# Optimization experiments

Measured on AMD Instinct MI355X. Metric: run time of the kernel, lower is better.

Reference implementation:

```python
import jax, jax.numpy as jnp
import numpy as np

B, H, W, C = 8, 64, 64, 512
DQK = C // 8  # query/key channel dim from Conv2D(filters//8, 1)


def setup_inputs() -> dict:
    key = jax.random.key(0)
    ks = jax.random.split(key, 8)
    s_in = 1.0 / np.sqrt(C)
    x = jax.random.normal(ks[0], (B, H, W, C), dtype=jnp.float32)
    Wq = jax.random.normal(ks[1], (C, DQK), dtype=jnp.float32) * s_in
    bq = jnp.zeros((DQK,), dtype=jnp.float32)
    Wk = jax.random.normal(ks[2], (C, DQK), dtype=jnp.float32) * s_in
    bk = jnp.zeros((DQK,), dtype=jnp.float32)
    Wv = jax.random.normal(ks[3], (C, C), dtype=jnp.float32) * s_in
    bv = jnp.zeros((C,), dtype=jnp.float32)
    # gamma initialized to zeros in the original, but use a nonzero value so
    # the attention branch actually contributes to the output/gradients.
    gamma = jnp.ones((1,), dtype=jnp.float32) * 0.5
    return {"x": x, "Wq": Wq, "bq": bq, "Wk": Wk, "bk": bk,
            "Wv": Wv, "bv": bv, "gamma": gamma}


def reference(x, Wq, bq, Wk, bk, Wv, bv, gamma):
    b, h, w, c = x.shape
    n = h * w  # spatial_size
    xf = x.reshape(b, n, c)
    # 1x1 convs == per-pixel channel matmuls
    q = xf @ Wq + bq            # [B, N, C//8]
    k = xf @ Wk + bk            # [B, N, C//8]
    v = xf @ Wv + bv            # [B, N, C]
    # Dot(axes=-1): attn[b,i,j] = sum_d q[b,i,d] * k[b,j,d]
    attn = jnp.einsum('bid,bjd->bij', q, k)
    attn = jax.nn.softmax(attn, axis=-1)
    # Dot(axes=-2): out[b,j,c] = sum_i attn[b,i,j] * v[b,i,c]  (note transpose)
    out = jnp.einsum('bij,bic->bjc', attn, v)
    out = out.reshape(b, h, w, c)
    return gamma * out + x
```

## Files before the change

### kernel.cpp

```cpp
#include <hip/hip_runtime.h>
#include <hip/hip_bf16.h>
#include <cstdio>

typedef unsigned short u16;
typedef __attribute__((ext_vector_type(4))) float f32x4;
typedef __attribute__((ext_vector_type(8))) short s16x8;

__device__ __forceinline__ u16 bf16b(float f) {
  union { float f; unsigned u; } c; c.f = f;
  unsigned u = c.u;
  return (u16)((u + 0x7FFFu + ((u >> 16) & 1u)) >> 16);
}

__device__ __forceinline__ void load16(const void* g, void* l) {
  __builtin_amdgcn_global_load_lds(
      (const __attribute__((address_space(1))) void*)g,
      (__attribute__((address_space(3))) void*)l, 16, 0, 0);
}

#define BARV() asm volatile("s_waitcnt vmcnt(0) lgkmcnt(0)\n\ts_barrier" ::: "memory")
#define BAR() asm volatile("s_waitcnt lgkmcnt(0)\n\ts_barrier" ::: "memory")


__global__ __launch_bounds__(256) void cvt_all_k(const float* __restrict__ x,
                                                 const float* __restrict__ Wq,
                                                 const float* __restrict__ Wk,
                                                 const float* __restrict__ Wv,
                                                 u16* __restrict__ xb,
                                                 u16* __restrict__ Wcat) {
  int bid = blockIdx.x;
  if (bid < 16384) {
    long i = ((long)bid * 256 + threadIdx.x) * 4;
    float4 f = *(const float4*)&x[i];
    unsigned lo = (unsigned)bf16b(f.x) | ((unsigned)bf16b(f.y) << 16);
    unsigned hi = (unsigned)bf16b(f.z) | ((unsigned)bf16b(f.w) << 16);
    uint2 v; v.x = lo; v.y = hi;
    *(uint2*)&xb[i] = v;
  } else {
    int idx = (bid - 16384) * 256 + threadIdx.x;
    int nn = idx >> 9, k = idx & 511;
    float v;
    if (nn < 64)       v = Wq[k * 64 + nn];
    else if (nn < 128) v = Wk[k * 64 + (nn - 64)];
    else               v = Wv[k * 512 + (nn - 128)];
    Wcat[idx] = bf16b(v);
  }
}

__global__ __launch_bounds__(256, 2) void projGemm(
    const u16* __restrict__ A, const u16* __restrict__ B,
    u16* __restrict__ Qb, u16* __restrict__ Kb, u16* __restrict__ Vt,
    const float* __restrict__ bq, const float* __restrict__ bk,
    const float* __restrict__ bv) {
  constexpr int BM = 128, BN = 128, FM = 4, FN = 4;
  __shared__ __align__(16) u16 At[BM * 64];
  __shared__ __align__(16) u16 Bt[BN * 64];
  const int tid = threadIdx.x;
  const int lane = tid & 63, w = tid >> 6;
  const int wr = w >> 1, wc = w & 1;
  const int l15 = lane & 15, lhi = lane >> 4;
  const long m0 = (long)blockIdx.x * BM;
  const long n0 = (long)blockIdx.y * BN;

  f32x4 acc[FM][FN] = {};

  for (int k0 = 0; k0 < 512; k0 += 64) {
#pragma unroll
    for (int it = 0; it < 8; ++it) {
      int q = it * 256 + tid;
      if (q < BM * 8) {
        int row = q >> 3, c8 = q & 7;
        load16(A + (m0 + row) * 512 + k0 + c8 * 8, &At[q * 8]);
      } else {
        int q2 = q - BM * 8;
        int row = q2 >> 3, c8 = q2 & 7;
        load16(B + (n0 + row) * 512 + k0 + c8 * 8, &Bt[q2 * 8]);
      }
    }
    __syncthreads();
#pragma unroll
    for (int kk = 0; kk < 64; kk += 32) {
      s16x8 af[FM], bf[FN];
#pragma unroll
      for (int i = 0; i < FM; ++i)
        af[i] = *(const s16x8*)&At[(wr * 64 + i * 16 + l15) * 64 + kk + lhi * 8];
#pragma unroll
      for (int j = 0; j < FN; ++j)
        bf[j] = *(const s16x8*)&Bt[(wc * 64 + j * 16 + l15) * 64 + kk + lhi * 8];
#pragma unroll
      for (int i = 0; i < FM; ++i)
#pragma unroll
        for (int j = 0; j < FN; ++j)
          acc[i][j] = __builtin_amdgcn_mfma_f32_16x16x32_bf16(af[i], bf[j],
                                                              acc[i][j], 0, 0, 0);
    }
    __syncthreads();
  }

#pragma unroll
  for (int i = 0; i < FM; ++i) {
#pragma unroll
    for (int j = 0; j < FN; ++j) {
      long mm = m0 + wr * 64 + i * 16 + lhi * 4;
      long nn = n0 + wc * 64 + j * 16 + l15;
      if (nn < 64) {
        float bb = bq[nn];
#pragma unroll
        for (int r = 0; r < 4; ++r)
          Qb[(mm + r) * 64 + nn] = bf16b(acc[i][j][r] + bb);
      } else if (nn < 128) {
        float bb = bk[nn - 64];
#pragma unroll
        for (int r = 0; r < 4; ++r)
          Kb[(mm + r) * 64 + nn - 64] = bf16b(acc[i][j][r] + bb);
      } else {
        long c = nn - 128;
        float bb = bv[c];
        unsigned u01 = (unsigned)bf16b(acc[i][j][0] + bb) |
                       ((unsigned)bf16b(acc[i][j][1] + bb) << 16);
        unsigned u23 = (unsigned)bf16b(acc[i][j][2] + bb) |
                       ((unsigned)bf16b(acc[i][j][3] + bb) << 16);
        uint2 u; u.x = u01; u.y = u23;
        *(uint2*)&Vt[(mm >> 12) * 512 * 4096 + c * 4096 + (mm & 4095)] = u;
      }
    }
  }
}

__global__ __launch_bounds__(256, 2) void stats_k(const u16* __restrict__ Qb,
                                                  const u16* __restrict__ Kb,
                                                  float* __restrict__ m_part,
                                                  float* __restrict__ l_part) {
  const int b = blockIdx.z, jc = blockIdx.y;
  const long i0 = (long)blockIdx.x * 128;
  const u16* Q = Qb + (long)b * 4096 * 64;
  const u16* Kp = Kb + (long)b * 4096 * 64;
  __shared__ __align__(16) u16 Qt[128 * 64];
  __shared__ __align__(16) u16 Kt[128 * 64];
  const int tid = threadIdx.x, lane = tid & 63, w = tid >> 6;
  const int l15 = lane & 15, lhi = lane >> 4;

#pragma unroll
  for (int it = 0; it < 4; ++it) {
    int q = it * 256 + tid;
    int row = q >> 3, c8 = q & 7;
    load16(Q + (i0 + row) * 64 + c8 * 8, &Qt[q * 8]);
  }

  float mrun[2][4], lrun[2][4];
#pragma unroll
  for (int i = 0; i < 2; ++i)
#pragma unroll
    for (int r = 0; r < 4; ++r) { mrun[i][r] = -1e30f; lrun[i][r] = 0.f; }

  for (int jt = 0; jt < 8; ++jt) {
    long j0 = (long)jc * 1024 + jt * 128;
#pragma unroll
    for (int it = 0; it < 4; ++it) {
      int q = it * 256 + tid;
      int row = q >> 3, c8 = q & 7;
      load16(Kp + (j0 + row) * 64 + c8 * 8, &Kt[q * 8]);
    }
    __syncthreads();
    f32x4 acc[2][8] = {};
#pragma unroll
    for (int kk = 0; kk < 64; kk += 32) {
      s16x8 af[2], bf[8];
#pragma unroll
      for (int i = 0; i < 2; ++i)
        af[i] = *(const s16x8*)&Qt[(w * 32 + i * 16 + l15) * 64 + kk + lhi * 8];
#pragma unroll
      for (int j = 0; j < 8; ++j)
        bf[j] = *(const s16x8*)&Kt[(j * 16 + l15) * 64 + kk + lhi * 8];
#pragma unroll
      for (int i = 0; i < 2; ++i)
#pragma unroll
        for (int j = 0; j < 8; ++j)
          acc[i][j] = __builtin_amdgcn_mfma_f32_16x16x32_bf16(af[i], bf[j],
                                                              acc[i][j], 0, 0, 0);
    }
#pragma unroll
    for (int i = 0; i < 2; ++i)
#pragma unroll
      for (int r = 0; r < 4; ++r) {
        float tm = acc[i][0][r];
#pragma unroll
        for (int j = 1; j < 8; ++j) tm = fmaxf(tm, acc[i][j][r]);
        float mo = mrun[i][r];
        float mn = fmaxf(mo, tm);
        float s = 0.f;
#pragma unroll
        for (int j = 0; j < 8; ++j) s += __expf(acc[i][j][r] - mn);
        lrun[i][r] = lrun[i][r] * __expf(mo - mn) + s;
        mrun[i][r] = mn;
      }
    __syncthreads();
  }

#pragma unroll
  for (int i = 0; i < 2; ++i)
#pragma unroll
    for (int r = 0; r < 4; ++r) {
      float m = mrun[i][r], l = lrun[i][r];
#pragma unroll
      for (int d = 1; d < 16; d <<= 1) {
        float mo = __shfl_xor(m, d);
        float lo = __shfl_xor(l, d);
        float mn = fmaxf(m, mo);
        l = l * __expf(m - mn) + lo * __expf(mo - mn);
        m = mn;
      }
      if (l15 == 0) {
        long ig = i0 + w * 32 + i * 16 + lhi * 4 + r;
        long idx = ((long)(b * 4 + jc)) * 4096 + ig;
        m_part[idx] = m;
        l_part[idx] = l;
      }
    }
}

__global__ __launch_bounds__(256) void merge_k(const float* __restrict__ m_part,
                                               const float* __restrict__ l_part,
                                               float* __restrict__ mfin,
                                               float* __restrict__ linv) {
  int idx = blockIdx.x * 256 + threadIdx.x;
  int b = idx >> 12, i = idx & 4095;
  float m = -1e30f, l = 0.f;
#pragma unroll
  for (int jc = 0; jc < 4; ++jc) {
    long o = ((long)(b * 4 + jc)) * 4096 + i;
    float mp = m_part[o], lp = l_part[o];
    float mn = fmaxf(m, mp);
    l = l * __expf(m - mn) + lp * __expf(mp - mn);
    m = mn;
  }
  mfin[idx] = m;
  linv[idx] = 1.0f / l;
}

__global__ __launch_bounds__(512, 2) void fusedPV(
    const u16* __restrict__ Qb, const u16* __restrict__ Kb,
    const u16* __restrict__ Vt, const float* __restrict__ mfin,
    const float* __restrict__ lnv, const float* __restrict__ x,
    const float* __restrict__ gamma, float* __restrict__ out) {
  __shared__ __align__(16) u16 Qc[2][64 * 64];
  __shared__ __align__(16) u16 Vc[2][256 * 64];
  __shared__ __align__(16) u16 Pl[256 * 64];
  const int tid = threadIdx.x, lane = tid & 63, w = tid >> 6;
  const int l15 = lane & 15, lhi = lane >> 4;
  const int wi = w & 1, wj = w >> 1, wc = w & 1;
  const int s = blockIdx.x + 16 * (blockIdx.y + 2 * blockIdx.z);
  const int pi = (s & 7) * 32 + (s >> 3);
  const int b = pi >> 5;
  const long j0 = (long)(pi & 15) * 256;
  const long c0 = (long)((pi >> 4) & 1) * 256;
  const u16* Qg = Qb + (long)b * 4096 * 64;
  const u16* Kg = Kb + (long)b * 4096 * 64;
  const u16* Vg = Vt + (long)b * 512 * 4096;
  const float* mg = mfin + (long)b * 4096;
  const float* lg = lnv + (long)b * 4096;

#pragma unroll
  for (int p = 0; p < 4; ++p) {
    int q = p * 512 + tid;
    int r = q >> 3, col = q & 7, cg = col ^ (r & 7);
    load16(Kg + (j0 + r) * 64 + cg * 8, (char*)Pl + r * 128 + col * 16);
  }
  BARV();
  s16x8 kf[4][2];
#pragma unroll
  for (int fj = 0; fj < 4; ++fj)
#pragma unroll
    for (int kx = 0; kx < 2; ++kx) {
      int r = wj * 64 + fj * 16 + l15;
      kf[fj][kx] = *(const s16x8*)((const char*)Pl + r * 128 +
                                   (((kx * 32 + lhi * 8) * 2) ^ ((r & 7) << 4)));
    }
  __syncthreads();

  {
    int r = tid >> 3, col = tid & 7, cg = col ^ (r & 7);
    load16(Qg + (long)r * 64 + cg * 8, (char*)&Qc[0][0] + r * 128 + col * 16);
#pragma unroll
    for (int p = 0; p < 4; ++p) {
      int q = p * 512 + tid;
      int r2 = q >> 3, c2 = q & 7, cg2 = c2 ^ (r2 & 7);
      load16(Vg + (c0 + r2) * 4096 + cg2 * 8,
             (char*)&Vc[0][0] + r2 * 128 + c2 * 16);
    }
  }

  f32x4 acc2[4][8] = {};
  const float gma = gamma[0];
  int cur = 0;

  for (int t = 0; t < 64; ++t) {
    const int i_base = t * 64;
    BARV();
    if (t < 63) {
      const long ib2 = (long)(t + 1) * 64;
      int r = tid >> 3, col = tid & 7, cg = col ^ (r & 7);
      load16(Qg + (ib2 + r) * 64 + cg * 8,
             (char*)&Qc[cur ^ 1][0] + r * 128 + col * 16);
#pragma unroll
      for (int p = 0; p < 4; ++p) {
        int q = p * 512 + tid;
        int r2 = q >> 3, c2 = q & 7, cg2 = c2 ^ (r2 & 7);
        load16(Vg + (c0 + r2) * 4096 + ib2 + cg2 * 8,
               (char*)&Vc[cur ^ 1][0] + r2 * 128 + c2 * 16);
      }
    }

    f32x4 acc1[2][4] = {};
#pragma unroll
    for (int kx = 0; kx < 2; ++kx) {
      s16x8 af[2];
#pragma unroll
      for (int fi = 0; fi < 2; ++fi) {
        int r = wi * 32 + fi * 16 + l15;
        af[fi] = *(const s16x8*)((const char*)&Qc[cur][0] + r * 128 +
                                 (((kx * 32 + lhi * 8) * 2) ^ ((r & 7) << 4)));
      }
#pragma unroll
      for (int fi = 0; fi < 2; ++fi)
#pragma unroll
        for (int fj = 0; fj < 4; ++fj)
          acc1[fi][fj] = __builtin_amdgcn_mfma_f32_16x16x32_bf16(
              af[fi], kf[fj][kx], acc1[fi][fj], 0, 0, 0);
    }

#pragma unroll
    for (int fi = 0; fi < 2; ++fi) {
      int i0l = wi * 32 + fi * 16 + lhi * 4;
      f32x4 mv = *(const f32x4*)&mg[i_base + i0l];
      f32x4 lv = *(const f32x4*)&lg[i_base + i0l];
#pragma unroll
      for (int fj = 0; fj < 4; ++fj) {
        int j = wj * 64 + fj * 16 + l15;
        float p0 = __expf(acc1[fi][fj][0] - mv[0]) * lv[0];
        float p1 = __expf(acc1[fi][fj][1] - mv[1]) * lv[1];
        float p2 = __expf(acc1[fi][fj][2] - mv[2]) * lv[2];
        float p3 = __expf(acc1[fi][fj][3] - mv[3]) * lv[3];
        unsigned u01 = (unsigned)bf16b(p0) | ((unsigned)bf16b(p1) << 16);
        unsigned u23 = (unsigned)bf16b(p2) | ((unsigned)bf16b(p3) << 16);
        char* base = (char*)Pl + j * 128;
        int byt = (i0l * 2) ^ ((j & 7) << 4);
        *(unsigned*)(base + byt) = u01;
        *(unsigned*)(base + byt + 4) = u23;
      }
    }
    BAR();

#pragma unroll
    for (int kx = 0; kx < 2; ++kx) {
      int kk = kx * 32;
      s16x8 pa[4];
#pragma unroll
      for (int fm = 0; fm < 4; ++fm) {
        int r = wj * 64 + fm * 16 + l15;
        pa[fm] = *(const s16x8*)((const char*)Pl + r * 128 +
                                 (((kk + lhi * 8) * 2) ^ ((r & 7) << 4)));
      }
#pragma unroll
      for (int fn = 0; fn < 8; ++fn) {
        int r = wc * 128 + fn * 16 + l15;
        s16x8 vb = *(const s16x8*)((const char*)&Vc[cur][0] + r * 128 +
                                   (((kk + lhi * 8) * 2) ^ ((r & 7) << 4)));
#pragma unroll
        for (int fm = 0; fm < 4; ++fm)
          acc2[fm][fn] = __builtin_amdgcn_mfma_f32_16x16x32_bf16(
              pa[fm], vb, acc2[fm][fn], 0, 0, 0);
      }
    }
    cur ^= 1;
  }

#pragma unroll
  for (int fm = 0; fm < 4; ++fm) {
#pragma unroll
    for (int fn = 0; fn < 8; ++fn) {
      long j = j0 + wj * 64 + fm * 16 + lhi * 4;
      long c = c0 + wc * 128 + fn * 16 + l15;
#pragma unroll
      for (int r = 0; r < 4; ++r) {
        long o = ((long)b * 4096 + j + r) * 512 + c;
        out[o] = gma * acc2[fm][fn][r] + x[o];
      }
    }
  }
}


extern "C" void kernel_launch(void* const* d_in, const int* in_sizes, int n_in,
                              void* d_out, int out_size, void* d_ws,
                              size_t ws_size, hipStream_t stream) {
  const float* x = (const float*)d_in[0];
  const float* Wq = (const float*)d_in[1];
  const float* bq = (const float*)d_in[2];
  const float* Wk = (const float*)d_in[3];
  const float* bk = (const float*)d_in[4];
  const float* Wv = (const float*)d_in[5];
  const float* bv = (const float*)d_in[6];
  const float* gamma = (const float*)d_in[7];
  float* out = (float*)d_out;

  char* ws = (char*)d_ws;
  size_t off = 0;
  auto alloc = [&](size_t bytes) {
    char* p = ws + off;
    off += (bytes + 255) & ~(size_t)255;
    return p;
  };
  u16* xb = (u16*)alloc((size_t)32768 * 512 * 2);
  u16* Wcat = (u16*)alloc((size_t)640 * 512 * 2);
  u16* Qb = (u16*)alloc((size_t)8 * 4096 * 64 * 2);
  u16* Kb = (u16*)alloc((size_t)8 * 4096 * 64 * 2);
  u16* Vt = (u16*)alloc((size_t)8 * 512 * 4096 * 2);
  float* m_part = (float*)alloc((size_t)8 * 4 * 4096 * 4);
  float* l_part = (float*)alloc((size_t)8 * 4 * 4096 * 4);
  float* mfin = (float*)alloc((size_t)8 * 4096 * 4);
  float* lnv = (float*)alloc((size_t)8 * 4096 * 4);
  if (off > ws_size) {
    fprintf(stderr, "kernel_launch: ws too small: need %zu have %zu\n", off,
            ws_size);
    return;
  }

  cvt_all_k<<<16384 + 1280, 256, 0, stream>>>(x, Wq, Wk, Wv, xb, Wcat);
  projGemm<<<dim3(256, 5, 1), 256, 0, stream>>>(xb, Wcat, Qb, Kb, Vt, bq, bk,
                                                bv);
  stats_k<<<dim3(32, 4, 8), 256, 0, stream>>>(Qb, Kb, m_part, l_part);
  merge_k<<<128, 256, 0, stream>>>(m_part, l_part, mfin, lnv);
  fusedPV<<<dim3(16, 2, 8), 512, 0, stream>>>(Qb, Kb, Vt, mfin, lnv, x,
                                              gamma, out);
}
```

Baseline: 324.0 us.

## Retile fusedPV to 64-row j tiles with register-staged V prefetch

Restructures the fused P·V kernel from 512-thread blocks covering 256 j-rows to 256-thread blocks covering 64 j-rows, which gives four times as many blocks and targets three blocks per CU. Q fragments now load straight from global memory into registers and are double-buffered by unrolling the loop by two. V tiles are prefetched through registers into a single LDS buffer instead of async global-to-LDS double buffering. MFMA phases get raised wave priority. This improves parallelism and occupancy, but each block recomputes QK^T and the exponentials for a smaller j tile, so that work is repeated about four times as often relative to the P·V work.

```diff
diff --git a/kernel.cpp b/kernel.cpp
--- a/kernel.cpp
+++ b/kernel.cpp
@@ -18,7 +18,6 @@
       (__attribute__((address_space(3))) void*)l, 16, 0, 0);
 }
 
-#define BARV() asm volatile("s_waitcnt vmcnt(0) lgkmcnt(0)\n\ts_barrier" ::: "memory")
 #define BAR() asm volatile("s_waitcnt lgkmcnt(0)\n\ts_barrier" ::: "memory")
 
 
@@ -238,149 +237,143 @@
   linv[idx] = 1.0f / l;
 }
 
-__global__ __launch_bounds__(512, 2) void fusedPV(
+#define PV_STEP(T, QFC, QFN)                                                   \
+  {                                                                            \
+    const int i_base = (T) * 64;                                               \
+    const int tnx = ((T) + 1) & 63;                                            \
+    _Pragma("unroll")                                                          \
+    for (int p = 0; p < 8; ++p) {                                              \
+      int q = p * 256 + tid; int r = q >> 3, col = q & 7;                      \
+      vreg[p] = *(const uint4*)&Vg[(long)r * 4096 + tnx * 64 + col * 8];       \
+    }                                                                          \
+    _Pragma("unroll")                                                          \
+    for (int fi = 0; fi < 2; ++fi)                                             \
+      _Pragma("unroll")                                                        \
+      for (int kx = 0; kx < 2; ++kx)                                           \
+        QFN[fi][kx] = *(const s16x8*)&Qg[(long)(tnx * 64 + wi * 32 + fi * 16 + \
+                                                l15) * 64 + kx * 32 + lhi * 8];\
+    f32x4 acc1[2][2] = {};                                                     \
+    _Pragma("unroll")                                                          \
+    for (int kx = 0; kx < 2; ++kx)                                             \
+      _Pragma("unroll")                                                        \
+      for (int fi = 0; fi < 2; ++fi)                                           \
+        _Pragma("unroll")                                                      \
+        for (int fj = 0; fj < 2; ++fj)                                         \
+          acc1[fi][fj] = __builtin_amdgcn_mfma_f32_16x16x32_bf16(              \
+              QFC[fi][kx], kf[fj][kx], acc1[fi][fj], 0, 0, 0);                 \
+    _Pragma("unroll")                                                          \
+    for (int fi = 0; fi < 2; ++fi) {                                           \
+      int i0l = wi * 32 + fi * 16 + lhi * 4;                                   \
+      f32x4 mv = *(const f32x4*)&mg[i_base + i0l];                             \
+      f32x4 lv = *(const f32x4*)&lg[i_base + i0l];                             \
+      _Pragma("unroll")                                                        \
+      for (int fj = 0; fj < 2; ++fj) {                                         \
+        int j = wjj * 32 + fj * 16 + l15;                                      \
+        float p0 = __expf(acc1[fi][fj][0] - mv[0]) * lv[0];                    \
+        float p1 = __expf(acc1[fi][fj][1] - mv[1]) * lv[1];                    \
+        float p2 = __expf(acc1[fi][fj][2] - mv[2]) * lv[2];                    \
+        float p3 = __expf(acc1[fi][fj][3] - mv[3]) * lv[3];                    \
+        uint2 u;                                                               \
+        u.x = (unsigned)bf16b(p0) | ((unsigned)bf16b(p1) << 16);               \
+        u.y = (unsigned)bf16b(p2) | ((unsigned)bf16b(p3) << 16);               \
+        *(uint2*)((char*)Pl + j * 128 + ((i0l * 2) ^ ((j & 7) << 4))) = u;     \
+      }                                                                        \
+    }                                                                          \
+    BAR();                                                                     \
+    __builtin_amdgcn_s_setprio(1);                                             \
+    _Pragma("unroll")                                                          \
+    for (int kx = 0; kx < 2; ++kx) {                                           \
+      s16x8 pa[4];                                                             \
+      _Pragma("unroll")                                                        \
+      for (int fm = 0; fm < 4; ++fm) {                                         \
+        int pr = fm * 16 + l15;                                                \
+        pa[fm] = *(const s16x8*)((const char*)Pl + pr * 128 +                  \
+                                 (((kx * 32 + lhi * 8) * 2) ^                  \
+                                  ((pr & 7) << 4)));                           \
+      }                                                                        \
+      _Pragma("unroll")                                                        \
+      for (int fn = 0; fn < 4; ++fn) {                                         \
+        int vr = w * 64 + fn * 16 + l15;                                       \
+        s16x8 vb = *(const s16x8*)((const char*)Vc + vr * 128 +                \
+                                   (((kx * 32 + lhi * 8) * 2) ^                \
+                                    ((vr & 7) << 4)));                         \
+        _Pragma("unroll")                                                      \
+        for (int fm = 0; fm < 4; ++fm)                                         \
+          acc2[fm][fn] = __builtin_amdgcn_mfma_f32_16x16x32_bf16(              \
+              pa[fm], vb, acc2[fm][fn], 0, 0, 0);                              \
+      }                                                                        \
+    }                                                                          \
+    __builtin_amdgcn_s_setprio(0);                                             \
+    BAR();                                                                     \
+    _Pragma("unroll")                                                          \
+    for (int p = 0; p < 8; ++p) {                                              \
+      int q = p * 256 + tid; int r = q >> 3, col = q & 7;                      \
+      *(uint4*)((char*)Vc + r * 128 + ((col * 16) ^ ((r & 7) << 4))) = vreg[p];\
+    }                                                                          \
+  }
+
+__global__ __launch_bounds__(256, 3) void fusedPV(
     const u16* __restrict__ Qb, const u16* __restrict__ Kb,
     const u16* __restrict__ Vt, const float* __restrict__ mfin,
     const float* __restrict__ lnv, const float* __restrict__ x,
     const float* __restrict__ gamma, float* __restrict__ out) {
-  __shared__ __align__(16) u16 Qc[2][64 * 64];
-  __shared__ __align__(16) u16 Vc[2][256 * 64];
-  __shared__ __align__(16) u16 Pl[256 * 64];
+  __shared__ __align__(16) u16 Vc[256 * 64];
+  __shared__ __align__(16) u16 Pl[64 * 64];
   const int tid = threadIdx.x, lane = tid & 63, w = tid >> 6;
   const int l15 = lane & 15, lhi = lane >> 4;
-  const int wi = w & 1, wj = w >> 1, wc = w & 1;
-  const int s = blockIdx.x + 16 * (blockIdx.y + 2 * blockIdx.z);
-  const int pi = (s & 7) * 32 + (s >> 3);
-  const int b = pi >> 5;
-  const long j0 = (long)(pi & 15) * 256;
-  const long c0 = (long)((pi >> 4) & 1) * 256;
+  const int wi = w & 1, wjj = w >> 1;
+  const int s = blockIdx.x + 64 * blockIdx.y + 128 * blockIdx.z;
+  const int pi = (s & 7) * 128 + (s >> 3);
+  const int b = pi >> 7;
+  const long c0 = (long)((pi >> 6) & 1) * 256;
+  const long j0 = (long)(pi & 63) * 64;
   const u16* Qg = Qb + (long)b * 4096 * 64;
   const u16* Kg = Kb + (long)b * 4096 * 64;
-  const u16* Vg = Vt + (long)b * 512 * 4096;
+  const u16* Vg = Vt + (long)b * 512 * 4096 + c0 * 4096;
   const float* mg = mfin + (long)b * 4096;
   const float* lg = lnv + (long)b * 4096;
-
-#pragma unroll
-  for (int p = 0; p < 4; ++p) {
-    int q = p * 512 + tid;
-    int r = q >> 3, col = q & 7, cg = col ^ (r & 7);
-    load16(Kg + (j0 + r) * 64 + cg * 8, (char*)Pl + r * 128 + col * 16);
-  }
-  BARV();
-  s16x8 kf[4][2];
-#pragma unroll
-  for (int fj = 0; fj < 4; ++fj)
-#pragma unroll
-    for (int kx = 0; kx < 2; ++kx) {
-      int r = wj * 64 + fj * 16 + l15;
-      kf[fj][kx] = *(const s16x8*)((const char*)Pl + r * 128 +
-                                   (((kx * 32 + lhi * 8) * 2) ^ ((r & 7) << 4)));
-    }
-  __syncthreads();
-
-  {
-    int r = tid >> 3, col = tid & 7, cg = col ^ (r & 7);
-    load16(Qg + (long)r * 64 + cg * 8, (char*)&Qc[0][0] + r * 128 + col * 16);
-#pragma unroll
-    for (int p = 0; p < 4; ++p) {
-      int q = p * 512 + tid;
-      int r2 = q >> 3, c2 = q & 7, cg2 = c2 ^ (r2 & 7);
-      load16(Vg + (c0 + r2) * 4096 + cg2 * 8,
-             (char*)&Vc[0][0] + r2 * 128 + c2 * 16);
-    }
-  }
-
-  f32x4 acc2[4][8] = {};
   const float gma = gamma[0];
-  int cur = 0;
-
-  for (int t = 0; t < 64; ++t) {
-    const int i_base = t * 64;
-    BARV();
-    if (t < 63) {
-      const long ib2 = (long)(t + 1) * 64;
-      int r = tid >> 3, col = tid & 7, cg = col ^ (r & 7);
-      load16(Qg + (ib2 + r) * 64 + cg * 8,
-             (char*)&Qc[cur ^ 1][0] + r * 128 + col * 16);
-#pragma unroll
-      for (int p = 0; p < 4; ++p) {
-        int q = p * 512 + tid;
-        int r2 = q >> 3, c2 = q & 7, cg2 = c2 ^ (r2 & 7);
-        load16(Vg + (c0 + r2) * 4096 + ib2 + cg2 * 8,
-               (char*)&Vc[cur ^ 1][0] + r2 * 128 + c2 * 16);
-      }
-    }
-
-    f32x4 acc1[2][4] = {};
-#pragma unroll
-    for (int kx = 0; kx < 2; ++kx) {
-      s16x8 af[2];
-#pragma unroll
-      for (int fi = 0; fi < 2; ++fi) {
-        int r = wi * 32 + fi * 16 + l15;
-        af[fi] = *(const s16x8*)((const char*)&Qc[cur][0] + r * 128 +
-                                 (((kx * 32 + lhi * 8) * 2) ^ ((r & 7) << 4)));
-      }
-#pragma unroll
-      for (int fi = 0; fi < 2; ++fi)
-#pragma unroll
-        for (int fj = 0; fj < 4; ++fj)
-          acc1[fi][fj] = __builtin_amdgcn_mfma_f32_16x16x32_bf16(
-              af[fi], kf[fj][kx], acc1[fi][fj], 0, 0, 0);
-    }
-
-#pragma unroll
-    for (int fi = 0; fi < 2; ++fi) {
-      int i0l = wi * 32 + fi * 16 + lhi * 4;
-      f32x4 mv = *(const f32x4*)&mg[i_base + i0l];
-      f32x4 lv = *(const f32x4*)&lg[i_base + i0l];
-#pragma unroll
-      for (int fj = 0; fj < 4; ++fj) {
-        int j = wj * 64 + fj * 16 + l15;
-        float p0 = __expf(acc1[fi][fj][0] - mv[0]) * lv[0];
-        float p1 = __expf(acc1[fi][fj][1] - mv[1]) * lv[1];
-        float p2 = __expf(acc1[fi][fj][2] - mv[2]) * lv[2];
-        float p3 = __expf(acc1[fi][fj][3] - mv[3]) * lv[3];
-        unsigned u01 = (unsigned)bf16b(p0) | ((unsigned)bf16b(p1) << 16);
-        unsigned u23 = (unsigned)bf16b(p2) | ((unsigned)bf16b(p3) << 16);
-        char* base = (char*)Pl + j * 128;
-        int byt = (i0l * 2) ^ ((j & 7) << 4);
-        *(unsigned*)(base + byt) = u01;
-        *(unsigned*)(base + byt + 4) = u23;
-      }
-    }
-    BAR();
-
-#pragma unroll
-    for (int kx = 0; kx < 2; ++kx) {
-      int kk = kx * 32;
-      s16x8 pa[4];
-#pragma unroll
-      for (int fm = 0; fm < 4; ++fm) {
-        int r = wj * 64 + fm * 16 + l15;
-        pa[fm] = *(const s16x8*)((const char*)Pl + r * 128 +
-                                 (((kk + lhi * 8) * 2) ^ ((r & 7) << 4)));
-      }
-#pragma unroll
-      for (int fn = 0; fn < 8; ++fn) {
-        int r = wc * 128 + fn * 16 + l15;
-        s16x8 vb = *(const s16x8*)((const char*)&Vc[cur][0] + r * 128 +
-                                   (((kk + lhi * 8) * 2) ^ ((r & 7) << 4)));
-#pragma unroll
-        for (int fm = 0; fm < 4; ++fm)
-          acc2[fm][fn] = __builtin_amdgcn_mfma_f32_16x16x32_bf16(
-              pa[fm], vb, acc2[fm][fn], 0, 0, 0);
-      }
-    }
-    cur ^= 1;
+
+  s16x8 kf[2][2];
+#pragma unroll
+  for (int fj = 0; fj < 2; ++fj)
+#pragma unroll
+    for (int kx = 0; kx < 2; ++kx)
+      kf[fj][kx] = *(const s16x8*)&Kg[(j0 + wjj * 32 + fj * 16 + l15) * 64 +
+                                      kx * 32 + lhi * 8];
+
+  uint4 vreg[8];
+  s16x8 qfA[2][2], qfB[2][2];
+#pragma unroll
+  for (int p = 0; p < 8; ++p) {
+    int q = p * 256 + tid; int r = q >> 3, col = q & 7;
+    vreg[p] = *(const uint4*)&Vg[(long)r * 4096 + col * 8];
+  }
+#pragma unroll
+  for (int fi = 0; fi < 2; ++fi)
+#pragma unroll
+    for (int kx = 0; kx < 2; ++kx)
+      qfA[fi][kx] = *(const s16x8*)&Qg[(long)(wi * 32 + fi * 16 + l15) * 64 +
+                                       kx * 32 + lhi * 8];
+#pragma unroll
+  for (int p = 0; p < 8; ++p) {
+    int q = p * 256 + tid; int r = q >> 3, col = q & 7;
+    *(uint4*)((char*)Vc + r * 128 + ((col * 16) ^ ((r & 7) << 4))) = vreg[p];
+  }
+
+  f32x4 acc2[4][4] = {};
+
+  for (int t = 0; t < 64; t += 2) {
+    PV_STEP(t, qfA, qfB);
+    PV_STEP(t + 1, qfB, qfA);
   }
 
 #pragma unroll
   for (int fm = 0; fm < 4; ++fm) {
 #pragma unroll
-    for (int fn = 0; fn < 8; ++fn) {
-      long j = j0 + wj * 64 + fm * 16 + lhi * 4;
-      long c = c0 + wc * 128 + fn * 16 + l15;
+    for (int fn = 0; fn < 4; ++fn) {
+      long j = j0 + fm * 16 + lhi * 4;
+      long c = c0 + w * 64 + fn * 16 + l15;
 #pragma unroll
       for (int r = 0; r < 4; ++r) {
         long o = ((long)b * 4096 + j + r) * 512 + c;
@@ -431,6 +424,6 @@
                                                 bv);
   stats_k<<<dim3(32, 4, 8), 256, 0, stream>>>(Qb, Kb, m_part, l_part);
   merge_k<<<128, 256, 0, stream>>>(m_part, l_part, mfin, lnv);
-  fusedPV<<<dim3(16, 2, 8), 512, 0, stream>>>(Qb, Kb, Vt, mfin, lnv, x,
+  fusedPV<<<dim3(64, 2, 8), 256, 0, stream>>>(Qb, Kb, Vt, mfin, lnv, x,
                                               gamma, out);
 }
```

Result: slower. 968.2 us (+198.8%).

## Shrink fusedPV tiles to 128 columns, drop double buffering, add setprio

Applied to the files above, without the earlier changes.

fusedPV now uses 256-thread blocks that each own 128 output rows j instead of 256, so the launch has twice as many blocks. The Q/V double buffer is replaced by a single buffer loaded synchronously at the top of each iteration, which cuts LDS use and should let more blocks fit per CU. s_setprio is raised around the PV MFMA section so co-resident waves can overlap loads with compute. In exchange, each block re-reads the full Q and V tiles for half the output work, and loads are no longer overlapped within a block.

```diff
diff --git a/kernel.cpp b/kernel.cpp
--- a/kernel.cpp
+++ b/kernel.cpp
@@ -17,9 +17,6 @@
       (const __attribute__((address_space(1))) void*)g,
       (__attribute__((address_space(3))) void*)l, 16, 0, 0);
 }
-
-#define BARV() asm volatile("s_waitcnt vmcnt(0) lgkmcnt(0)\n\ts_barrier" ::: "memory")
-#define BAR() asm volatile("s_waitcnt lgkmcnt(0)\n\ts_barrier" ::: "memory")
 
 
 __global__ __launch_bounds__(256) void cvt_all_k(const float* __restrict__ x,
@@ -238,35 +235,36 @@
   linv[idx] = 1.0f / l;
 }
 
-__global__ __launch_bounds__(512, 2) void fusedPV(
+__global__ __launch_bounds__(256, 2) void fusedPV(
     const u16* __restrict__ Qb, const u16* __restrict__ Kb,
     const u16* __restrict__ Vt, const float* __restrict__ mfin,
     const float* __restrict__ lnv, const float* __restrict__ x,
     const float* __restrict__ gamma, float* __restrict__ out) {
-  __shared__ __align__(16) u16 Qc[2][64 * 64];
-  __shared__ __align__(16) u16 Vc[2][256 * 64];
-  __shared__ __align__(16) u16 Pl[256 * 64];
+  __shared__ __align__(16) u16 Qc[64 * 64];
+  __shared__ __align__(16) u16 Vc[256 * 64];
+  __shared__ __align__(16) u16 Pl[128 * 64];
   const int tid = threadIdx.x, lane = tid & 63, w = tid >> 6;
   const int l15 = lane & 15, lhi = lane >> 4;
   const int wi = w & 1, wj = w >> 1, wc = w & 1;
-  const int s = blockIdx.x + 16 * (blockIdx.y + 2 * blockIdx.z);
-  const int pi = (s & 7) * 32 + (s >> 3);
-  const int b = pi >> 5;
-  const long j0 = (long)(pi & 15) * 256;
-  const long c0 = (long)((pi >> 4) & 1) * 256;
+  const int s = blockIdx.x + 32 * (blockIdx.y + 2 * blockIdx.z);
+  const int pi = (s & 7) * 64 + (s >> 3);
+  const int b = pi >> 6;
+  const long c0 = (long)((pi >> 5) & 1) * 256;
+  const long j0 = (long)(pi & 31) * 128;
   const u16* Qg = Qb + (long)b * 4096 * 64;
   const u16* Kg = Kb + (long)b * 4096 * 64;
   const u16* Vg = Vt + (long)b * 512 * 4096;
   const float* mg = mfin + (long)b * 4096;
   const float* lg = lnv + (long)b * 4096;
+  const float gma = gamma[0];
 
 #pragma unroll
   for (int p = 0; p < 4; ++p) {
-    int q = p * 512 + tid;
+    int q = p * 256 + tid;
     int r = q >> 3, col = q & 7, cg = col ^ (r & 7);
     load16(Kg + (j0 + r) * 64 + cg * 8, (char*)Pl + r * 128 + col * 16);
   }
-  BARV();
+  asm volatile("s_waitcnt vmcnt(0) lgkmcnt(0)\n\ts_barrier" ::: "memory");
   s16x8 kf[4][2];
 #pragma unroll
   for (int fj = 0; fj < 4; ++fj)
@@ -278,38 +276,25 @@
     }
   __syncthreads();
 
-  {
-    int r = tid >> 3, col = tid & 7, cg = col ^ (r & 7);
-    load16(Qg + (long)r * 64 + cg * 8, (char*)&Qc[0][0] + r * 128 + col * 16);
-#pragma unroll
-    for (int p = 0; p < 4; ++p) {
-      int q = p * 512 + tid;
-      int r2 = q >> 3, c2 = q & 7, cg2 = c2 ^ (r2 & 7);
-      load16(Vg + (c0 + r2) * 4096 + cg2 * 8,
-             (char*)&Vc[0][0] + r2 * 128 + c2 * 16);
-    }
-  }
-
   f32x4 acc2[4][8] = {};
-  const float gma = gamma[0];
-  int cur = 0;
 
   for (int t = 0; t < 64; ++t) {
     const int i_base = t * 64;
-    BARV();
-    if (t < 63) {
-      const long ib2 = (long)(t + 1) * 64;
-      int r = tid >> 3, col = tid & 7, cg = col ^ (r & 7);
-      load16(Qg + (ib2 + r) * 64 + cg * 8,
-             (char*)&Qc[cur ^ 1][0] + r * 128 + col * 16);
-#pragma unroll
-      for (int p = 0; p < 4; ++p) {
-        int q = p * 512 + tid;
-        int r2 = q >> 3, c2 = q & 7, cg2 = c2 ^ (r2 & 7);
-        load16(Vg + (c0 + r2) * 4096 + ib2 + cg2 * 8,
-               (char*)&Vc[cur ^ 1][0] + r2 * 128 + c2 * 16);
-      }
-    }
+#pragma unroll
+    for (int p = 0; p < 2; ++p) {
+      int q = p * 256 + tid;
+      int r = q >> 3, col = q & 7, cg = col ^ (r & 7);
+      load16(Qg + (long)(i_base + r) * 64 + cg * 8,
+             (char*)Qc + r * 128 + col * 16);
+    }
+#pragma unroll
+    for (int p = 0; p < 8; ++p) {
+      int q = p * 256 + tid;
+      int r = q >> 3, col = q & 7, cg = col ^ (r & 7);
+      load16(Vg + (c0 + r) * 4096 + i_base + cg * 8,
+             (char*)Vc + r * 128 + col * 16);
+    }
+    __syncthreads();
 
     f32x4 acc1[2][4] = {};
 #pragma unroll
@@ -318,7 +303,7 @@
 #pragma unroll
       for (int fi = 0; fi < 2; ++fi) {
         int r = wi * 32 + fi * 16 + l15;
-        af[fi] = *(const s16x8*)((const char*)&Qc[cur][0] + r * 128 +
+        af[fi] = *(const s16x8*)((const char*)Qc + r * 128 +
                                  (((kx * 32 + lhi * 8) * 2) ^ ((r & 7) << 4)));
       }
 #pragma unroll
@@ -341,16 +326,15 @@
         float p1 = __expf(acc1[fi][fj][1] - mv[1]) * lv[1];
         float p2 = __expf(acc1[fi][fj][2] - mv[2]) * lv[2];
         float p3 = __expf(acc1[fi][fj][3] - mv[3]) * lv[3];
-        unsigned u01 = (unsigned)bf16b(p0) | ((unsigned)bf16b(p1) << 16);
-        unsigned u23 = (unsigned)bf16b(p2) | ((unsigned)bf16b(p3) << 16);
-        char* base = (char*)Pl + j * 128;
-        int byt = (i0l * 2) ^ ((j & 7) << 4);
-        *(unsigned*)(base + byt) = u01;
-        *(unsigned*)(base + byt + 4) = u23;
-      }
-    }
-    BAR();
-
+        uint2 u;
+        u.x = (unsigned)bf16b(p0) | ((unsigned)bf16b(p1) << 16);
+        u.y = (unsigned)bf16b(p2) | ((unsigned)bf16b(p3) << 16);
+        *(uint2*)((char*)Pl + j * 128 + ((i0l * 2) ^ ((j & 7) << 4))) = u;
+      }
+    }
+    __syncthreads();
+
+    __builtin_amdgcn_s_setprio(1);
 #pragma unroll
     for (int kx = 0; kx < 2; ++kx) {
       int kk = kx * 32;
@@ -364,7 +348,7 @@
 #pragma unroll
       for (int fn = 0; fn < 8; ++fn) {
         int r = wc * 128 + fn * 16 + l15;
-        s16x8 vb = *(const s16x8*)((const char*)&Vc[cur][0] + r * 128 +
+        s16x8 vb = *(const s16x8*)((const char*)Vc + r * 128 +
                                    (((kk + lhi * 8) * 2) ^ ((r & 7) << 4)));
 #pragma unroll
         for (int fm = 0; fm < 4; ++fm)
@@ -372,7 +356,8 @@
               pa[fm], vb, acc2[fm][fn], 0, 0, 0);
       }
     }
-    cur ^= 1;
+    __builtin_amdgcn_s_setprio(0);
+    __syncthreads();
   }
 
 #pragma unroll
@@ -431,6 +416,6 @@
                                                 bv);
   stats_k<<<dim3(32, 4, 8), 256, 0, stream>>>(Qb, Kb, m_part, l_part);
   merge_k<<<128, 256, 0, stream>>>(m_part, l_part, mfin, lnv);
-  fusedPV<<<dim3(16, 2, 8), 512, 0, stream>>>(Qb, Kb, Vt, mfin, lnv, x,
+  fusedPV<<<dim3(32, 2, 8), 256, 0, stream>>>(Qb, Kb, Vt, mfin, lnv, x,
                                               gamma, out);
 }
```

Measured after the change: 304.6 us. 1.06x faster.
